# Kernel optimization log

Hardware: AMD Instinct MI355X
Metric: run time of the kernel (lower is better)

## Reference

```python
import jax, jax.numpy as jnp
import numpy as np

NODE_V = 16  # node_vocab_size
EDGE_V = 8   # edge_vocab_size
B, N = 64, 256


def _encode_single(x, vocab_size):
    # round to integer bucket, map bucket centers to (-1, 1)
    return 2.0 * ((jnp.round(x) + 0.5) / vocab_size) - 1.0


def setup_inputs() -> dict:
    key = jax.random.key(0)
    k1, k2, k3 = jax.random.split(key, 3)
    x_nodes = jax.random.uniform(k1, (B, N, 1), dtype=jnp.float32, minval=0.0, maxval=float(NODE_V))
    x_edges = jax.random.uniform(k2, (B, N, N), dtype=jnp.float32, minval=0.0, maxval=float(EDGE_V))
    g_0 = jax.random.normal(k3, (B,), dtype=jnp.float32)
    return {"x_nodes": x_nodes, "x_edges": x_edges, "g_0": g_0}


def reference(x_nodes, x_edges, g_0):
    # encode: quantize continuous inputs to bucket centers in (-1, 1)
    zn = _encode_single(x_nodes, NODE_V)  # [b, n, 1]
    ze = _encode_single(x_edges, EDGE_V)  # [b, n, n]

    # codebook values for each vocab bucket, also mapped to (-1, 1)
    node_vals = _encode_single(jnp.arange(NODE_V, dtype=jnp.float32), NODE_V)  # [Vn]
    edge_vals = _encode_single(jnp.arange(EDGE_V, dtype=jnp.float32), EDGE_V)  # [Ve]

    inv_stdev = jnp.exp(-0.5 * g_0)  # [b]

    # decode nodes: [b, n, 1] - [Vn] -> [b, n, Vn]
    node_logits = -0.5 * jnp.square((zn - node_vals) * inv_stdev[:, None, None])
    node_logprobs = jax.nn.log_softmax(node_logits, axis=-1)

    # decode edges: [b, n, n, 1] - [Ve] -> [b, n, n, Ve]
    edge_logits = -0.5 * jnp.square((ze[..., None] - edge_vals) * inv_stdev[:, None, None, None])
    edge_logprobs = jax.nn.log_softmax(edge_logits, axis=-1)

    return node_logprobs, edge_logprobs
```

## Files before the change

### kernel.cpp

```cpp
#include <hip/hip_runtime.h>
#include <hip/hip_bf16.h>

#define NODE_V 16
#define EDGE_V 8
#define BATCH  64
#define NSEQ   256

#define EDGE_ELEMS  (BATCH * NSEQ * NSEQ)
#define EDGE_BLOCKS (EDGE_ELEMS / 1024)
#define NODE_OUT_FLOATS ((size_t)BATCH * NSEQ * NODE_V)

__global__ __launch_bounds__(256) void fused_kernel(const float* __restrict__ xn,
                                                    const float* __restrict__ xe,
                                                    const float* __restrict__ g0,
                                                    float* __restrict__ out) {
    if (blockIdx.x < EDGE_BLOCKS) {
        __shared__ __align__(16) float tbl[9 * 12];
        const int blk = blockIdx.x;
        const int b   = blk >> 6;

        if (threadIdx.x < 9) {
            const float inv = expf(-0.5f * g0[b]);
            const int bucket = threadIdx.x;
            const float z = 2.0f * ((float)bucket + 0.5f) / (float)EDGE_V - 1.0f;
            float l[EDGE_V];
            float m = -1e30f;
            #pragma unroll
            for (int v = 0; v < EDGE_V; ++v) {
                const float ev = 2.0f * ((float)v + 0.5f) / (float)EDGE_V - 1.0f;
                const float d  = (z - ev) * inv;
                l[v] = -0.5f * d * d;
                m = fmaxf(m, l[v]);
            }
            float s = 0.0f;
            #pragma unroll
            for (int v = 0; v < EDGE_V; ++v) s += expf(l[v] - m);
            const float lse = m + logf(s);
            #pragma unroll
            for (int v = 0; v < EDGE_V; ++v) tbl[bucket * 12 + v] = l[v] - lse;
        }
        __syncthreads();

        const float4* t4 = (const float4*)tbl;
        float4* o4 = (float4*)(out + NODE_OUT_FLOATS);
        const size_t qbase = (size_t)blk * 2048;
        #pragma unroll
        for (int r = 0; r < 8; ++r) {
            const size_t q = qbase + (size_t)(r * 256 + threadIdx.x);
            const float x = xe[q >> 1];
            const int bucket = (int)rintf(x);
            o4[q] = t4[bucket * 3 + (int)(q & 1)];
        }
    } else {
        __shared__ __align__(16) float tbl[17 * 20];
        const int b = blockIdx.x - EDGE_BLOCKS;

        if (threadIdx.x < 17) {
            const float inv = expf(-0.5f * g0[b]);
            const int bucket = threadIdx.x;
            const float z = 2.0f * ((float)bucket + 0.5f) / (float)NODE_V - 1.0f;
            float l[NODE_V];
            float m = -1e30f;
            #pragma unroll
            for (int v = 0; v < NODE_V; ++v) {
                const float ev = 2.0f * ((float)v + 0.5f) / (float)NODE_V - 1.0f;
                const float d  = (z - ev) * inv;
                l[v] = -0.5f * d * d;
                m = fmaxf(m, l[v]);
            }
            float s = 0.0f;
            #pragma unroll
            for (int v = 0; v < NODE_V; ++v) s += expf(l[v] - m);
            const float lse = m + logf(s);
            #pragma unroll
            for (int v = 0; v < NODE_V; ++v) tbl[bucket * 20 + v] = l[v] - lse;
        }
        __syncthreads();

        const float4* t4 = (const float4*)tbl;
        float4* o4 = (float4*)out;
        const size_t qbase = (size_t)b * 1024;
        #pragma unroll
        for (int r = 0; r < 4; ++r) {
            const int q = r * 256 + threadIdx.x;
            const float x = xn[b * NSEQ + (q >> 2)];
            const int bucket = (int)rintf(x);
            o4[qbase + q] = t4[bucket * 5 + (q & 3)];
        }
    }
}

extern "C" void kernel_launch(void* const* d_in, const int* in_sizes, int n_in,
                              void* d_out, int out_size, void* d_ws, size_t ws_size,
                              hipStream_t stream) {
    const float* xn = (const float*)d_in[0];
    const float* xe = (const float*)d_in[1];
    const float* g0 = (const float*)d_in[2];
    float* out = (float*)d_out;

    fused_kernel<<<dim3(EDGE_BLOCKS + BATCH), dim3(256), 0, stream>>>(xn, xe, g0, out);
}
```

Measured before the change: 28.66 us.

## Double edge elements per block, parallelize table softmax via shuffles, use nontemporal stores

Each edge block now handles 2048 elements instead of 1024, halving the edge block count and the per-block table setup. The per-batch log-softmax table is built with one thread per entry and wavefront shuffle reductions instead of a serial loop in a few threads, shortening the prologue before the barrier. Output writes use nontemporal stores so the large streaming output skips cache retention. Risks: fewer blocks means less parallelism to hide latency, and nontemporal stores may behave differently on this memory hierarchy.

```diff
diff --git a/kernel.cpp b/kernel.cpp
--- a/kernel.cpp
+++ b/kernel.cpp
@@ -7,85 +7,88 @@
 #define NSEQ   256
 
 #define EDGE_ELEMS  (BATCH * NSEQ * NSEQ)
-#define EDGE_BLOCKS (EDGE_ELEMS / 1024)
+#define EPB         2048
+#define EDGE_BLOCKS (EDGE_ELEMS / EPB)
+#define BLKS_PER_B  (NSEQ * NSEQ / EPB)
 #define NODE_OUT_FLOATS ((size_t)BATCH * NSEQ * NODE_V)
+
+typedef float f32x4 __attribute__((ext_vector_type(4)));
 
 __global__ __launch_bounds__(256) void fused_kernel(const float* __restrict__ xn,
                                                     const float* __restrict__ xe,
                                                     const float* __restrict__ g0,
                                                     float* __restrict__ out) {
+    const int tid = threadIdx.x;
     if (blockIdx.x < EDGE_BLOCKS) {
         __shared__ __align__(16) float tbl[9 * 12];
         const int blk = blockIdx.x;
-        const int b   = blk >> 6;
+        const int b   = blk / BLKS_PER_B;
 
-        if (threadIdx.x < 9) {
+        if (tid < 72) {
             const float inv = expf(-0.5f * g0[b]);
-            const int bucket = threadIdx.x;
-            const float z = 2.0f * ((float)bucket + 0.5f) / (float)EDGE_V - 1.0f;
-            float l[EDGE_V];
-            float m = -1e30f;
+            const int bucket = tid >> 3;
+            const int v      = tid & 7;
+            const float z  = 2.0f * ((float)bucket + 0.5f) / (float)EDGE_V - 1.0f;
+            const float ev = 2.0f * ((float)v + 0.5f) / (float)EDGE_V - 1.0f;
+            const float d  = (z - ev) * inv;
+            const float l  = -0.5f * d * d;
+            float m = l;
             #pragma unroll
-            for (int v = 0; v < EDGE_V; ++v) {
-                const float ev = 2.0f * ((float)v + 0.5f) / (float)EDGE_V - 1.0f;
-                const float d  = (z - ev) * inv;
-                l[v] = -0.5f * d * d;
-                m = fmaxf(m, l[v]);
-            }
-            float s = 0.0f;
+            for (int off = 1; off < 8; off <<= 1) m = fmaxf(m, __shfl_xor(m, off, 8));
+            float s = expf(l - m);
             #pragma unroll
-            for (int v = 0; v < EDGE_V; ++v) s += expf(l[v] - m);
-            const float lse = m + logf(s);
-            #pragma unroll
-            for (int v = 0; v < EDGE_V; ++v) tbl[bucket * 12 + v] = l[v] - lse;
+            for (int off = 1; off < 8; off <<= 1) s += __shfl_xor(s, off, 8);
+            tbl[bucket * 12 + v] = l - m - logf(s);
         }
         __syncthreads();
 
-        const float4* t4 = (const float4*)tbl;
-        float4* o4 = (float4*)(out + NODE_OUT_FLOATS);
-        const size_t qbase = (size_t)blk * 2048;
+        const f32x4* t4 = (const f32x4*)tbl;
+        f32x4* o4 = (f32x4*)(out + NODE_OUT_FLOATS);
+        const size_t qbase = (size_t)blk * (EPB * 2);
         #pragma unroll
-        for (int r = 0; r < 8; ++r) {
-            const size_t q = qbase + (size_t)(r * 256 + threadIdx.x);
+        for (int r = 0; r < EPB * 2 / 256; ++r) {
+            const size_t q = qbase + (size_t)(r * 256 + tid);
             const float x = xe[q >> 1];
             const int bucket = (int)rintf(x);
-            o4[q] = t4[bucket * 3 + (int)(q & 1)];
+            const f32x4 val = t4[bucket * 3 + (int)(q & 1)];
+            __builtin_nontemporal_store(val, &o4[q]);
         }
     } else {
         __shared__ __align__(16) float tbl[17 * 20];
         const int b = blockIdx.x - EDGE_BLOCKS;
 
-        if (threadIdx.x < 17) {
-            const float inv = expf(-0.5f * g0[b]);
-            const int bucket = threadIdx.x;
-            const float z = 2.0f * ((float)bucket + 0.5f) / (float)NODE_V - 1.0f;
-            float l[NODE_V];
-            float m = -1e30f;
-            #pragma unroll
-            for (int v = 0; v < NODE_V; ++v) {
+        const float inv = expf(-0.5f * g0[b]);
+        #pragma unroll
+        for (int pass = 0; pass < 2; ++pass) {
+            const int e = pass * 256 + tid;
+            if (e < 17 * 16) {
+                const int bucket = e >> 4;
+                const int v      = e & 15;
+                const float z  = 2.0f * ((float)bucket + 0.5f) / (float)NODE_V - 1.0f;
                 const float ev = 2.0f * ((float)v + 0.5f) / (float)NODE_V - 1.0f;
                 const float d  = (z - ev) * inv;
-                l[v] = -0.5f * d * d;
-                m = fmaxf(m, l[v]);
+                const float l  = -0.5f * d * d;
+                float m = l;
+                #pragma unroll
+                for (int off = 1; off < 16; off <<= 1) m = fmaxf(m, __shfl_xor(m, off, 16));
+                float s = expf(l - m);
+                #pragma unroll
+                for (int off = 1; off < 16; off <<= 1) s += __shfl_xor(s, off, 16);
+                tbl[bucket * 20 + v] = l - m - logf(s);
             }
-            float s = 0.0f;
-            #pragma unroll
-            for (int v = 0; v < NODE_V; ++v) s += expf(l[v] - m);
-            const float lse = m + logf(s);
-            #pragma unroll
-            for (int v = 0; v < NODE_V; ++v) tbl[bucket * 20 + v] = l[v] - lse;
         }
         __syncthreads();
 
-        const float4* t4 = (const float4*)tbl;
-        float4* o4 = (float4*)out;
+        const f32x4* t4 = (const f32x4*)tbl;
+        f32x4* o4 = (f32x4*)out;
         const size_t qbase = (size_t)b * 1024;
         #pragma unroll
         for (int r = 0; r < 4; ++r) {
-            const int q = r * 256 + threadIdx.x;
+            const int q = r * 256 + tid;
             const float x = xn[b * NSEQ + (q >> 2)];
             const int bucket = (int)rintf(x);
-            o4[qbase + q] = t4[bucket * 5 + (q & 3)];
+            const f32x4 val = t4[bucket * 5 + (q & 3)];
+            __builtin_nontemporal_store(val, &o4[qbase + q]);
         }
     }
 }
```

Result: slower. 30.82 us (+7.5%).
